# Kernel tuning notes

Measured on AMD Instinct MI355X. Metric: run time of the kernel, lower is better.

## Reference

```python
import jax, jax.numpy as jnp
import numpy as np

N_NODES = 50000
N_EDGES = 800000
D_IN = 128
D_H = 128


def setup_inputs() -> dict:
    key = jax.random.key(0)
    ks = jax.random.split(key, 16)
    s = 0.05
    return {
        "x": jax.random.normal(ks[0], (N_NODES, D_IN), dtype=jnp.float32),
        "edge_index": jax.random.randint(ks[1], (2, N_EDGES), 0, N_NODES, dtype=jnp.int64),
        # GraphConv 1: out = aggr(x_j) @ W_rel + b + x @ W_root (lin_root has no bias in PyG)
        "W1_rel": jax.random.normal(ks[2], (D_IN, D_H), dtype=jnp.float32) * s,
        "b1": jnp.zeros((D_H,), dtype=jnp.float32),
        "W1_root": jax.random.normal(ks[3], (D_IN, D_H), dtype=jnp.float32) * s,
        # GraphConv 2
        "W2_rel": jax.random.normal(ks[4], (D_H, D_H), dtype=jnp.float32) * s,
        "b2": jnp.zeros((D_H,), dtype=jnp.float32),
        "W2_root": jax.random.normal(ks[5], (D_H, D_H), dtype=jnp.float32) * s,
        # mean head MLP: Linear(2H->H), ReLU, Linear(H->1)
        "Wm1": jax.random.normal(ks[6], (2 * D_H, D_H), dtype=jnp.float32) * s,
        "bm1": jnp.zeros((D_H,), dtype=jnp.float32),
        "Wm2": jax.random.normal(ks[7], (D_H, 1), dtype=jnp.float32) * s,
        "bm2": jnp.zeros((1,), dtype=jnp.float32),
        # logvar head MLP
        "Wv1": jax.random.normal(ks[8], (2 * D_H, D_H), dtype=jnp.float32) * s,
        "bv1": jnp.zeros((D_H,), dtype=jnp.float32),
        "Wv2": jax.random.normal(ks[9], (D_H, 1), dtype=jnp.float32) * s,
        "bv2": jnp.zeros((1,), dtype=jnp.float32),
    }


def _graph_conv(h, src, dst, n, W_rel, b, W_root):
    # PyG GraphConv (aggr='add'): out_i = (sum_{j->i} h_j) @ W_rel + b + h_i @ W_root
    agg = jax.ops.segment_sum(h[src], dst, num_segments=n)
    return agg @ W_rel + b + h @ W_root


def reference(x, edge_index, W1_rel, b1, W1_root, W2_rel, b2, W2_root,
              Wm1, bm1, Wm2, bm2, Wv1, bv1, Wv2, bv2):
    n = x.shape[0]
    src, dst = edge_index[0], edge_index[1]
    h = jax.nn.relu(_graph_conv(x, src, dst, n, W1_rel, b1, W1_root))
    h = jax.nn.relu(_graph_conv(h, src, dst, n, W2_rel, b2, W2_root))
    combined = jnp.concatenate([h[src], h[dst]], axis=1)  # [E, 2H]
    mean = jax.nn.relu(combined @ Wm1 + bm1) @ Wm2 + bm2  # [E, 1]
    logvar = jax.nn.relu(combined @ Wv1 + bv1) @ Wv2 + bv2
    var = jnp.exp(0.5 * logvar)
    return (mean, var)
```

## Files before the change

### kernel.cpp

```cpp
#include <hip/hip_runtime.h>
#include <cstdint>

#define NF 128

typedef unsigned int uint;
typedef short bf16x8 __attribute__((ext_vector_type(8)));
typedef float f32x4  __attribute__((ext_vector_type(4)));

__device__ __forceinline__ float2 ld2(const float* p) {
    return *reinterpret_cast<const float2*>(p);
}
__device__ __forceinline__ float bflo(uint u) { return __uint_as_float(u << 16); }
__device__ __forceinline__ float bfhi(uint u) { return __uint_as_float(u & 0xffff0000u); }
__device__ __forceinline__ uint f2bf_rne(float f) {
    uint u = __float_as_uint(f);
    return (u + 0x7fffu + ((u >> 16) & 1u)) >> 16;
}
__device__ __forceinline__ uint pack2bf(float a, float b) {
    return f2bf_rne(a) | (f2bf_rne(b) << 16);
}

__device__ __forceinline__ bf16x8 ldfrag(const uint* __restrict__ tab, int idx, int kb, int g) {
    const uint4 u = *reinterpret_cast<const uint4*>(&tab[(size_t)idx * 64 + kb * 16 + g * 4]);
    union { uint4 u4; bf16x8 b; } c; c.u4 = u; return c.b;
}

__global__ __launch_bounds__(256) void cast_bf16_k(const float* __restrict__ in,
                                                   uint* __restrict__ out, int npairs)
{
    int i = blockIdx.x * 256 + threadIdx.x;
    if (i >= npairs) return;
    float2 v = ld2(&in[(size_t)i * 2]);
    out[i] = pack2bf(v.x, v.y);
}

struct W8 {
    const float* src[8];
    uint*        dst[8];
};
__global__ __launch_bounds__(256) void wtpack_k(W8 p)
{
    int m = blockIdx.y;
    const float* s = p.src[m];
    uint* d = p.dst[m];
    int idx = blockIdx.x * 256 + threadIdx.x;
    int c   = idx >> 6;
    int kdw = idx & 63;
    float a = s[(size_t)(2 * kdw)     * NF + c];
    float b = s[(size_t)(2 * kdw + 1) * NF + c];
    d[(size_t)c * 64 + kdw] = pack2bf(a, b);
}

__global__ __launch_bounds__(256) void count_k(const int* __restrict__ ei,
                                               int* __restrict__ deg, int E)
{
    int e = blockIdx.x * 256 + threadIdx.x;
    if (e >= E) return;
    atomicAdd(&deg[ei[E + e]], 1);
}

__global__ __launch_bounds__(256) void scan1_k(const int* __restrict__ deg,
                                               int* __restrict__ rowptr,
                                               int* __restrict__ bsum, int N)
{
    int i = blockIdx.x * 256 + threadIdx.x;
    int v = (i < N) ? deg[i] : 0;
    int lane = threadIdx.x & 63;
    int wid  = threadIdx.x >> 6;
    int x = v;
#pragma unroll
    for (int off = 1; off < 64; off <<= 1) {
        int y = __shfl_up(x, off);
        if (lane >= off) x += y;
    }
    __shared__ int wsum[4];
    if (lane == 63) wsum[wid] = x;
    __syncthreads();
    int wadd = 0;
#pragma unroll
    for (int w = 0; w < 4; ++w) wadd += (w < wid) ? wsum[w] : 0;
    int incl = x + wadd;
    if (i < N) rowptr[i] = incl - v;
    if (threadIdx.x == 255) bsum[blockIdx.x] = incl;
}

__global__ __launch_bounds__(256) void scan2_k(int* __restrict__ bsum, int NB)
{
    int i = threadIdx.x;
    int v = (i < NB) ? bsum[i] : 0;
    int lane = threadIdx.x & 63;
    int wid  = threadIdx.x >> 6;
    int x = v;
#pragma unroll
    for (int off = 1; off < 64; off <<= 1) {
        int y = __shfl_up(x, off);
        if (lane >= off) x += y;
    }
    __shared__ int wsum[4];
    if (lane == 63) wsum[wid] = x;
    __syncthreads();
    int wadd = 0;
#pragma unroll
    for (int w = 0; w < 4; ++w) wadd += (w < wid) ? wsum[w] : 0;
    int incl = x + wadd;
    __syncthreads();
    if (i < NB) bsum[i] = incl - v;
}

__global__ __launch_bounds__(256) void scan3_k(const int* __restrict__ bsum,
                                               int* __restrict__ rowptr,
                                               int* __restrict__ cursor, int N, int E)
{
    int i = blockIdx.x * 256 + threadIdx.x;
    if (i == 0) rowptr[N] = E;
    if (i >= N) return;
    int r = rowptr[i] + bsum[blockIdx.x];
    rowptr[i] = r;
    cursor[i] = r;
}

__global__ __launch_bounds__(256) void fill_k(const int* __restrict__ ei,
                                              int* __restrict__ cursor,
                                              int* __restrict__ srclist,
                                              int* __restrict__ invpos, int E)
{
    int e = blockIdx.x * 256 + threadIdx.x;
    if (e >= E) return;
    int s = ei[e];
    int d = ei[E + e];
    int pos = atomicAdd(&cursor[d], 1);
    srclist[pos] = s;
    invpos[e] = pos;
}

__global__ __launch_bounds__(256) void agg2_k(const uint* __restrict__ Xb,
                                              const int* __restrict__ rowptr,
                                              const int* __restrict__ srclist,
                                              uint* __restrict__ AGGb, int N)
{
    int gid   = blockIdx.x * 256 + threadIdx.x;
    int wave  = gid >> 6;
    int lane  = gid & 63;
    int half  = lane >> 5;
    int hlane = lane & 31;
    int node  = wave * 2 + half;
    int nc    = min(node, N - 1);
    int beg = rowptr[nc];
    int end = rowptr[nc + 1];
    if (node >= N) { beg = 0; end = 0; }

    float ax = 0.f, ay = 0.f, az = 0.f, aw = 0.f;
    float bx = 0.f, by = 0.f, bz = 0.f, bw = 0.f;

    uint2 w0 = make_uint2(0, 0), w1 = make_uint2(0, 0);
    int ok1 = 0;
    if (beg < end) {
        int s0 = srclist[beg];
        ok1 = (beg + 1 < end);
        int s1 = ok1 ? srclist[beg + 1] : s0;
        w0 = *reinterpret_cast<const uint2*>(&Xb[(size_t)s0 * 64 + hlane * 2]);
        w1 = *reinterpret_cast<const uint2*>(&Xb[(size_t)s1 * 64 + hlane * 2]);
    }
    for (int j = beg; j < end; j += 2) {
        int jn = j + 2;
        uint2 nw0 = w0, nw1 = w1;
        int nok1 = 0;
        if (jn < end) {
            int s0 = srclist[jn];
            nok1 = (jn + 1 < end);
            int s1 = nok1 ? srclist[jn + 1] : s0;
            nw0 = *reinterpret_cast<const uint2*>(&Xb[(size_t)s0 * 64 + hlane * 2]);
            nw1 = *reinterpret_cast<const uint2*>(&Xb[(size_t)s1 * 64 + hlane * 2]);
        }
        ax += bflo(w0.x); ay += bfhi(w0.x); az += bflo(w0.y); aw += bfhi(w0.y);
        if (ok1) { bx += bflo(w1.x); by += bfhi(w1.x); bz += bflo(w1.y); bw += bfhi(w1.y); }
        w0 = nw0; w1 = nw1; ok1 = nok1;
    }
    if (node < N) {
        uint2 o;
        o.x = pack2bf(ax + bx, ay + by);
        o.y = pack2bf(az + bz, aw + bw);
        *reinterpret_cast<uint2*>(&AGGb[(size_t)node * 64 + hlane * 2]) = o;
    }
}

__global__ __launch_bounds__(256) void dualgemm_mfma_k(
    const uint* __restrict__ Aa, const uint* __restrict__ WaT,
    const uint* __restrict__ Ab, const uint* __restrict__ WbT,
    const float* __restrict__ bias, uint* __restrict__ C, int Nrows)
{
    const int lane = threadIdx.x & 63;
    const int wid  = threadIdx.x >> 6;
    const int g    = lane >> 4;
    const int r15  = lane & 15;
    const int rowBase = blockIdx.x * 128 + wid * 32;
    if (rowBase >= Nrows) return;
    const int arow0 = rowBase + r15;
    const int t1ok  = (rowBase + 16) < Nrows;
    const int arow1 = t1ok ? (rowBase + 16 + r15) : arow0;

    bf16x8 ba0[4], bb0[4], ba1[4], bb1[4];
#pragma unroll
    for (int kb = 0; kb < 4; ++kb) {
        ba0[kb] = ldfrag(Aa, arow0, kb, g);
        bb0[kb] = ldfrag(Ab, arow0, kb, g);
        ba1[kb] = ldfrag(Aa, arow1, kb, g);
        bb1[kb] = ldfrag(Ab, arow1, kb, g);
    }

#pragma unroll
    for (int ct = 0; ct < 8; ++ct) {
        const int wcol = ct * 16 + r15;
        f32x4 a0 = {0.f, 0.f, 0.f, 0.f};
        f32x4 a1 = {0.f, 0.f, 0.f, 0.f};
#pragma unroll
        for (int kb = 0; kb < 4; ++kb) {
            bf16x8 wf = ldfrag(WaT, wcol, kb, g);
            a0 = __builtin_amdgcn_mfma_f32_16x16x32_bf16(wf, ba0[kb], a0, 0, 0, 0);
            a1 = __builtin_amdgcn_mfma_f32_16x16x32_bf16(wf, ba1[kb], a1, 0, 0, 0);
        }
#pragma unroll
        for (int kb = 0; kb < 4; ++kb) {
            bf16x8 wf = ldfrag(WbT, wcol, kb, g);
            a0 = __builtin_amdgcn_mfma_f32_16x16x32_bf16(wf, bb0[kb], a0, 0, 0, 0);
            a1 = __builtin_amdgcn_mfma_f32_16x16x32_bf16(wf, bb1[kb], a1, 0, 0, 0);
        }

        const int colBase = ct * 16 + g * 4;
        float4 bs = *reinterpret_cast<const float4*>(&bias[colBase]);
        uint2 pk0, pk1;
        pk0.x = pack2bf(fmaxf(a0[0] + bs.x, 0.f), fmaxf(a0[1] + bs.y, 0.f));
        pk0.y = pack2bf(fmaxf(a0[2] + bs.z, 0.f), fmaxf(a0[3] + bs.w, 0.f));
        pk1.x = pack2bf(fmaxf(a1[0] + bs.x, 0.f), fmaxf(a1[1] + bs.y, 0.f));
        pk1.y = pack2bf(fmaxf(a1[2] + bs.z, 0.f), fmaxf(a1[3] + bs.w, 0.f));
        *reinterpret_cast<uint2*>(&C[(size_t)arow0 * 64 + ct * 8 + g * 2]) = pk0;
        if (t1ok)
            *reinterpret_cast<uint2*>(&C[(size_t)arow1 * 64 + ct * 8 + g * 2]) = pk1;
    }
}

__global__ __launch_bounds__(256) void headgemm_mfma_k(
    const uint* __restrict__ Hb,
    const uint* __restrict__ WPt, const uint* __restrict__ WQt,
    const uint* __restrict__ WRt, const uint* __restrict__ WSt,
    const float* __restrict__ bm1, const float* __restrict__ bv1,
    uint* __restrict__ PRb, uint* __restrict__ QSb, int Nrows)
{
    const int lane = threadIdx.x & 63;
    const int wid  = threadIdx.x >> 6;
    const int g    = lane >> 4;
    const int r15  = lane & 15;
    const int rowBase = blockIdx.x * 128 + wid * 32;
    if (rowBase >= Nrows) return;
    const int arow0 = rowBase + r15;
    const int t1ok  = (rowBase + 16) < Nrows;
    const int arow1 = t1ok ? (rowBase + 16 + r15) : arow0;

    bf16x8 hb0[4], hb1[4];
#pragma unroll
    for (int kb = 0; kb < 4; ++kb) {
        hb0[kb] = ldfrag(Hb, arow0, kb, g);
        hb1[kb] = ldfrag(Hb, arow1, kb, g);
    }

#pragma unroll
    for (int ct = 0; ct < 8; ++ct) {
        const int wcol = ct * 16 + r15;
        f32x4 aP0 = {0.f,0.f,0.f,0.f}, aQ0 = {0.f,0.f,0.f,0.f};
        f32x4 aR0 = {0.f,0.f,0.f,0.f}, aS0 = {0.f,0.f,0.f,0.f};
        f32x4 aP1 = {0.f,0.f,0.f,0.f}, aQ1 = {0.f,0.f,0.f,0.f};
        f32x4 aR1 = {0.f,0.f,0.f,0.f}, aS1 = {0.f,0.f,0.f,0.f};
#pragma unroll
        for (int kb = 0; kb < 4; ++kb) {
            bf16x8 wP = ldfrag(WPt, wcol, kb, g);
            bf16x8 wQ = ldfrag(WQt, wcol, kb, g);
            bf16x8 wR = ldfrag(WRt, wcol, kb, g);
            bf16x8 wS = ldfrag(WSt, wcol, kb, g);
            aP0 = __builtin_amdgcn_mfma_f32_16x16x32_bf16(wP, hb0[kb], aP0, 0, 0, 0);
            aP1 = __builtin_amdgcn_mfma_f32_16x16x32_bf16(wP, hb1[kb], aP1, 0, 0, 0);
            aQ0 = __builtin_amdgcn_mfma_f32_16x16x32_bf16(wQ, hb0[kb], aQ0, 0, 0, 0);
            aQ1 = __builtin_amdgcn_mfma_f32_16x16x32_bf16(wQ, hb1[kb], aQ1, 0, 0, 0);
            aR0 = __builtin_amdgcn_mfma_f32_16x16x32_bf16(wR, hb0[kb], aR0, 0, 0, 0);
            aR1 = __builtin_amdgcn_mfma_f32_16x16x32_bf16(wR, hb1[kb], aR1, 0, 0, 0);
            aS0 = __builtin_amdgcn_mfma_f32_16x16x32_bf16(wS, hb0[kb], aS0, 0, 0, 0);
            aS1 = __builtin_amdgcn_mfma_f32_16x16x32_bf16(wS, hb1[kb], aS1, 0, 0, 0);
        }
        const int colBase = ct * 16 + g * 4;
        float4 bmv = *reinterpret_cast<const float4*>(&bm1[colBase]);
        float4 bvv = *reinterpret_cast<const float4*>(&bv1[colBase]);
        uint4 pr0, qs0, pr1, qs1;
        pr0.x = pack2bf(aP0[0] + bmv.x, aP0[1] + bmv.y);
        pr0.y = pack2bf(aR0[0] + bvv.x, aR0[1] + bvv.y);
        pr0.z = pack2bf(aP0[2] + bmv.z, aP0[3] + bmv.w);
        pr0.w = pack2bf(aR0[2] + bvv.z, aR0[3] + bvv.w);
        qs0.x = pack2bf(aQ0[0], aQ0[1]); qs0.y = pack2bf(aS0[0], aS0[1]);
        qs0.z = pack2bf(aQ0[2], aQ0[3]); qs0.w = pack2bf(aS0[2], aS0[3]);
        pr1.x = pack2bf(aP1[0] + bmv.x, aP1[1] + bmv.y);
        pr1.y = pack2bf(aR1[0] + bvv.x, aR1[1] + bvv.y);
        pr1.z = pack2bf(aP1[2] + bmv.z, aP1[3] + bmv.w);
        pr1.w = pack2bf(aR1[2] + bvv.z, aR1[3] + bvv.w);
        qs1.x = pack2bf(aQ1[0], aQ1[1]); qs1.y = pack2bf(aS1[0], aS1[1]);
        qs1.z = pack2bf(aQ1[2], aQ1[3]); qs1.w = pack2bf(aS1[2], aS1[3]);
        *reinterpret_cast<uint4*>(&PRb[(size_t)arow0 * 128 + ct * 16 + g * 4]) = pr0;
        *reinterpret_cast<uint4*>(&QSb[(size_t)arow0 * 128 + ct * 16 + g * 4]) = qs0;
        if (t1ok) {
            *reinterpret_cast<uint4*>(&PRb[(size_t)arow1 * 128 + ct * 16 + g * 4]) = pr1;
            *reinterpret_cast<uint4*>(&QSb[(size_t)arow1 * 128 + ct * 16 + g * 4]) = qs1;
        }
    }
}

__global__ __launch_bounds__(256) void edge_head3_k(
    const uint* __restrict__ PRb, const uint* __restrict__ QSb,
    const int* __restrict__ rowptr, const int* __restrict__ srclist,
    const float* __restrict__ Wm2, const float* __restrict__ Wv2,
    float2* __restrict__ tmp, int N)
{
    int gid   = blockIdx.x * 256 + threadIdx.x;
    int node  = gid >> 6;
    int lane  = gid & 63;
    int half  = lane >> 5;
    int hlane = lane & 31;
    if (node >= N) return;
    int beg = rowptr[node];
    int end = rowptr[node + 1];
    if (beg == end) return;

    uint4 qs4 = *reinterpret_cast<const uint4*>(&QSb[(size_t)node * 128 + hlane * 4]);
    float q0 = bflo(qs4.x), q1 = bfhi(qs4.x);
    float s0 = bflo(qs4.y), s1 = bfhi(qs4.y);
    float q2 = bflo(qs4.z), q3 = bfhi(qs4.z);
    float s2 = bflo(qs4.w), s3 = bfhi(qs4.w);

    float4 wm = *reinterpret_cast<const float4*>(&Wm2[hlane * 4]);
    float4 wv = *reinterpret_cast<const float4*>(&Wv2[hlane * 4]);

    int p0 = beg + half;
    int src0 = srclist[min(p0, end - 1)];
    uint4 pr_cur = *reinterpret_cast<const uint4*>(&PRb[(size_t)src0 * 128 + hlane * 4]);

    for (int base = beg; base < end; base += 2) {
        int p = base + half;
        uint4 pr_next = pr_cur;
        if (base + 2 < end) {
            int pn = base + 2 + half;
            int srcn = srclist[min(pn, end - 1)];
            pr_next = *reinterpret_cast<const uint4*>(&PRb[(size_t)srcn * 128 + hlane * 4]);
        }

        float P0 = bflo(pr_cur.x), P1 = bfhi(pr_cur.x);
        float R0 = bflo(pr_cur.y), R1 = bfhi(pr_cur.y);
        float P2 = bflo(pr_cur.z), P3 = bfhi(pr_cur.z);
        float R2 = bflo(pr_cur.w), R3 = bfhi(pr_cur.w);

        float pm = fmaf(fmaxf(P0 + q0, 0.f), wm.x,
                   fmaf(fmaxf(P1 + q1, 0.f), wm.y,
                   fmaf(fmaxf(P2 + q2, 0.f), wm.z,
                        fmaxf(P3 + q3, 0.f) * wm.w)));
        float pv = fmaf(fmaxf(R0 + s0, 0.f), wv.x,
                   fmaf(fmaxf(R1 + s1, 0.f), wv.y,
                   fmaf(fmaxf(R2 + s2, 0.f), wv.z,
                        fmaxf(R3 + s3, 0.f) * wv.w)));

        pm += __shfl_xor(pm, 16);
        pv += __shfl_xor(pv, 16);
        float c = (hlane & 16) ? pv : pm;
        c += __shfl_xor(c, 8);
        c += __shfl_xor(c, 4);
        c += __shfl_xor(c, 2);
        c += __shfl_xor(c, 1);
        float other = __shfl(c, (lane & 32) + 16);
        if (hlane == 0 && p < end) tmp[p] = make_float2(c, other);

        pr_cur = pr_next;
    }
}

__global__ __launch_bounds__(256) void permute_k(
    const float2* __restrict__ tmp, const int* __restrict__ invpos,
    const float* __restrict__ bm2, const float* __restrict__ bv2,
    float* __restrict__ mean_out, float* __restrict__ var_out, int E)
{
    int e = blockIdx.x * 256 + threadIdx.x;
    if (e >= E) return;
    float2 t = tmp[invpos[e]];
    mean_out[e] = t.x + bm2[0];
    var_out[e]  = expf(0.5f * (t.y + bv2[0]));
}

extern "C" void kernel_launch(void* const* d_in, const int* in_sizes, int n_in,
                              void* d_out, int out_size, void* d_ws, size_t ws_size,
                              hipStream_t stream)
{
    const float* x       = (const float*)d_in[0];
    const int*   ei      = (const int*)d_in[1];
    const float* W1_rel  = (const float*)d_in[2];
    const float* b1      = (const float*)d_in[3];
    const float* W1_root = (const float*)d_in[4];
    const float* W2_rel  = (const float*)d_in[5];
    const float* b2      = (const float*)d_in[6];
    const float* W2_root = (const float*)d_in[7];
    const float* Wm1     = (const float*)d_in[8];
    const float* bm1     = (const float*)d_in[9];
    const float* Wm2     = (const float*)d_in[10];
    const float* bm2     = (const float*)d_in[11];
    const float* Wv1     = (const float*)d_in[12];
    const float* bv1     = (const float*)d_in[13];
    const float* Wv2     = (const float*)d_in[14];
    const float* bv2     = (const float*)d_in[15];

    const int N = in_sizes[0] / NF;
    const int E = in_sizes[1] / 2;

    const size_t SZ16 = (size_t)N * NF * 2;

    char* base = (char*)d_ws;
    uint* x_b  = (uint*)(base);
    uint* h2b  = (uint*)(base);
    uint* h1b  = (uint*)(base + SZ16);
    uint* AGGb = (uint*)(base + 2 * SZ16);
    uint* PRb  = (uint*)(base + SZ16);
    uint* QSb  = (uint*)(base + 3 * SZ16);

    char* wts = base + 5 * SZ16;
    uint* wt[8];
    for (int i = 0; i < 8; ++i) wt[i] = (uint*)(wts + (size_t)i * 32768);

    char* csr = wts + 8 * 32768;
    int* deg     = (int*)(csr);
    int* rowptr  = (int*)(csr + (size_t)(N + 64) * 4);
    int* cursor  = (int*)(csr + (size_t)(N + 64) * 8);
    int* srclist = (int*)(csr + (size_t)(N + 64) * 12);
    int* invpos  = srclist + E;
    float2* tmp  = (float2*)(invpos + E);
    int* bsum    = (int*)(tmp + E);

    float* out_mean = (float*)d_out;
    float* out_var  = out_mean + E;

    dim3 blk(256);
    dim3 eGrid((E + 255) / 256);
    dim3 mfmaGrid((N + 127) / 128);
    dim3 nodeGrid((unsigned)(((size_t)N * 64 + 255) / 256));
    dim3 node2Grid((unsigned)((((size_t)(N + 1) / 2) * 64 + 255) / 256));
    const int NB = (N + 255) / 256;
    dim3 scanGrid(NB);

    hipLaunchKernelGGL(cast_bf16_k, nodeGrid, blk, 0, stream, x, x_b, N * 64);

    W8 wp;
    wp.src[0] = W1_rel;            wp.dst[0] = wt[0];
    wp.src[1] = W1_root;           wp.dst[1] = wt[1];
    wp.src[2] = W2_rel;            wp.dst[2] = wt[2];
    wp.src[3] = W2_root;           wp.dst[3] = wt[3];
    wp.src[4] = Wm1;               wp.dst[4] = wt[4];
    wp.src[5] = Wm1 + NF * NF;     wp.dst[5] = wt[5];
    wp.src[6] = Wv1;               wp.dst[6] = wt[6];
    wp.src[7] = Wv1 + NF * NF;     wp.dst[7] = wt[7];
    hipLaunchKernelGGL(wtpack_k, dim3(32, 8), blk, 0, stream, wp);

    hipMemsetAsync(deg, 0, (size_t)N * 4, stream);
    hipLaunchKernelGGL(count_k, eGrid, blk, 0, stream, ei, deg, E);
    hipLaunchKernelGGL(scan1_k, scanGrid, blk, 0, stream, deg, rowptr, bsum, N);
    hipLaunchKernelGGL(scan2_k, dim3(1), blk, 0, stream, bsum, NB);
    hipLaunchKernelGGL(scan3_k, scanGrid, blk, 0, stream, bsum, rowptr, cursor, N, E);
    hipLaunchKernelGGL(fill_k, eGrid, blk, 0, stream, ei, cursor, srclist, invpos, E);

    hipLaunchKernelGGL(agg2_k, node2Grid, blk, 0, stream, x_b, rowptr, srclist, AGGb, N);
    hipLaunchKernelGGL(dualgemm_mfma_k, mfmaGrid, blk, 0, stream,
                       AGGb, wt[0], x_b, wt[1], b1, h1b, N);

    hipLaunchKernelGGL(agg2_k, node2Grid, blk, 0, stream, h1b, rowptr, srclist, AGGb, N);
    hipLaunchKernelGGL(dualgemm_mfma_k, mfmaGrid, blk, 0, stream,
                       AGGb, wt[2], h1b, wt[3], b2, h2b, N);

    hipLaunchKernelGGL(headgemm_mfma_k, mfmaGrid, blk, 0, stream,
                       h2b, wt[4], wt[5], wt[6], wt[7], bm1, bv1, PRb, QSb, N);

    hipLaunchKernelGGL(edge_head3_k, nodeGrid, blk, 0, stream,
                       PRb, QSb, rowptr, srclist, Wm2, Wv2, tmp, N);

    hipLaunchKernelGGL(permute_k, eGrid, blk, 0, stream,
                       tmp, invpos, bm2, bv2, out_mean, out_var, E);
}
```

Measured before the change: 450.4 us.

## Fuse prologue kernels, merge scan passes, and fuse conv2 GEMM into head GEMM

Merges the x cast, weight packing and degree counting into one prologue launch. The scan's second and third passes become one kernel in which each block recomputes its prefix from the block sums. The second GraphConv GEMM now keeps its bf16 output tile in LDS and feeds it straight into the head GEMM, so h2 is never written to or read back from global memory. This removes several launches and a full node-feature round trip, at the cost of more LDS per block and somewhat redundant per-block prefix sums.

```diff
diff --git a/kernel.cpp b/kernel.cpp
--- a/kernel.cpp
+++ b/kernel.cpp
@@ -25,38 +25,38 @@
     union { uint4 u4; bf16x8 b; } c; c.u4 = u; return c.b;
 }
 
-__global__ __launch_bounds__(256) void cast_bf16_k(const float* __restrict__ in,
-                                                   uint* __restrict__ out, int npairs)
-{
-    int i = blockIdx.x * 256 + threadIdx.x;
-    if (i >= npairs) return;
-    float2 v = ld2(&in[(size_t)i * 2]);
-    out[i] = pack2bf(v.x, v.y);
-}
-
 struct W8 {
     const float* src[8];
     uint*        dst[8];
 };
-__global__ __launch_bounds__(256) void wtpack_k(W8 p)
-{
-    int m = blockIdx.y;
-    const float* s = p.src[m];
-    uint* d = p.dst[m];
-    int idx = blockIdx.x * 256 + threadIdx.x;
-    int c   = idx >> 6;
-    int kdw = idx & 63;
-    float a = s[(size_t)(2 * kdw)     * NF + c];
-    float b = s[(size_t)(2 * kdw + 1) * NF + c];
-    d[(size_t)c * 64 + kdw] = pack2bf(a, b);
-}
-
-__global__ __launch_bounds__(256) void count_k(const int* __restrict__ ei,
-                                               int* __restrict__ deg, int E)
-{
-    int e = blockIdx.x * 256 + threadIdx.x;
-    if (e >= E) return;
-    atomicAdd(&deg[ei[E + e]], 1);
+__global__ __launch_bounds__(256) void prologue_k(
+    const float* __restrict__ x, uint* __restrict__ x_b, int npairs, int castBlocks,
+    W8 wp,
+    const int* __restrict__ ei, int* __restrict__ deg, int E, int countBlocks)
+{
+    int b = blockIdx.x;
+    if (b < castBlocks) {
+        int i = b * 256 + threadIdx.x;
+        if (i >= npairs) return;
+        float2 v = ld2(&x[(size_t)i * 2]);
+        x_b[i] = pack2bf(v.x, v.y);
+    } else if (b < castBlocks + 256) {
+        int wb = b - castBlocks;
+        int m  = wb >> 5;
+        int bx = wb & 31;
+        const float* s = wp.src[m];
+        uint* d = wp.dst[m];
+        int idx = bx * 256 + threadIdx.x;
+        int c   = idx >> 6;
+        int kdw = idx & 63;
+        float a  = s[(size_t)(2 * kdw)     * NF + c];
+        float b2 = s[(size_t)(2 * kdw + 1) * NF + c];
+        d[(size_t)c * 64 + kdw] = pack2bf(a, b2);
+    } else {
+        int e = (b - castBlocks - 256) * 256 + threadIdx.x;
+        if (e >= E) return;
+        atomicAdd(&deg[ei[E + e]], 1);
+    }
 }
 
 __global__ __launch_bounds__(256) void scan1_k(const int* __restrict__ deg,
@@ -84,37 +84,25 @@
     if (threadIdx.x == 255) bsum[blockIdx.x] = incl;
 }
 
-__global__ __launch_bounds__(256) void scan2_k(int* __restrict__ bsum, int NB)
-{
-    int i = threadIdx.x;
-    int v = (i < NB) ? bsum[i] : 0;
-    int lane = threadIdx.x & 63;
-    int wid  = threadIdx.x >> 6;
-    int x = v;
-#pragma unroll
-    for (int off = 1; off < 64; off <<= 1) {
-        int y = __shfl_up(x, off);
-        if (lane >= off) x += y;
-    }
-    __shared__ int wsum[4];
-    if (lane == 63) wsum[wid] = x;
+__global__ __launch_bounds__(256) void scan23_k(const int* __restrict__ bsum,
+                                                int* __restrict__ rowptr,
+                                                int* __restrict__ cursor, int N, int E)
+{
+    int tid = threadIdx.x;
+    int v = (tid < blockIdx.x) ? bsum[tid] : 0;
+    int lane = tid & 63;
+    int wid  = tid >> 6;
+#pragma unroll
+    for (int off = 32; off > 0; off >>= 1) v += __shfl_xor(v, off);
+    __shared__ int ws[4];
+    if (lane == 0) ws[wid] = v;
     __syncthreads();
-    int wadd = 0;
-#pragma unroll
-    for (int w = 0; w < 4; ++w) wadd += (w < wid) ? wsum[w] : 0;
-    int incl = x + wadd;
-    __syncthreads();
-    if (i < NB) bsum[i] = incl - v;
-}
-
-__global__ __launch_bounds__(256) void scan3_k(const int* __restrict__ bsum,
-                                               int* __restrict__ rowptr,
-                                               int* __restrict__ cursor, int N, int E)
-{
-    int i = blockIdx.x * 256 + threadIdx.x;
-    if (i == 0) rowptr[N] = E;
+    int prefix = ws[0] + ws[1] + ws[2] + ws[3];
+
+    if (blockIdx.x == 0 && tid == 0) rowptr[N] = E;
+    int i = blockIdx.x * 256 + tid;
     if (i >= N) return;
-    int r = rowptr[i] + bsum[blockIdx.x];
+    int r = rowptr[i] + prefix;
     rowptr[i] = r;
     cursor[i] = r;
 }
@@ -239,28 +227,78 @@
     }
 }
 
-__global__ __launch_bounds__(256) void headgemm_mfma_k(
-    const uint* __restrict__ Hb,
+#define LROW 72
+__global__ __launch_bounds__(256) void conv2head_k(
+    const uint* __restrict__ Aa, const uint* __restrict__ WaT,
+    const uint* __restrict__ Ab, const uint* __restrict__ WbT,
+    const float* __restrict__ bias,
     const uint* __restrict__ WPt, const uint* __restrict__ WQt,
     const uint* __restrict__ WRt, const uint* __restrict__ WSt,
     const float* __restrict__ bm1, const float* __restrict__ bv1,
     uint* __restrict__ PRb, uint* __restrict__ QSb, int Nrows)
 {
+    __shared__ uint h2s[128 * LROW];
+
     const int lane = threadIdx.x & 63;
     const int wid  = threadIdx.x >> 6;
     const int g    = lane >> 4;
     const int r15  = lane & 15;
     const int rowBase = blockIdx.x * 128 + wid * 32;
-    if (rowBase >= Nrows) return;
+    const int active = rowBase < Nrows;
     const int arow0 = rowBase + r15;
-    const int t1ok  = (rowBase + 16) < Nrows;
-    const int arow1 = t1ok ? (rowBase + 16 + r15) : arow0;
-
+    const int t1ok  = active && ((rowBase + 16) < Nrows);
+    const int arow1 = t1ok ? (rowBase + 16 + r15) : (active ? arow0 : 0);
+    const int lrow0 = wid * 32 + r15;
+    const int lrow1 = wid * 32 + 16 + r15;
+
+    if (active) {
+        bf16x8 ba0[4], bb0[4], ba1[4], bb1[4];
+#pragma unroll
+        for (int kb = 0; kb < 4; ++kb) {
+            ba0[kb] = ldfrag(Aa, arow0, kb, g);
+            bb0[kb] = ldfrag(Ab, arow0, kb, g);
+            ba1[kb] = ldfrag(Aa, arow1, kb, g);
+            bb1[kb] = ldfrag(Ab, arow1, kb, g);
+        }
+#pragma unroll
+        for (int ct = 0; ct < 8; ++ct) {
+            const int wcol = ct * 16 + r15;
+            f32x4 a0 = {0.f, 0.f, 0.f, 0.f};
+            f32x4 a1 = {0.f, 0.f, 0.f, 0.f};
+#pragma unroll
+            for (int kb = 0; kb < 4; ++kb) {
+                bf16x8 wf = ldfrag(WaT, wcol, kb, g);
+                a0 = __builtin_amdgcn_mfma_f32_16x16x32_bf16(wf, ba0[kb], a0, 0, 0, 0);
+                a1 = __builtin_amdgcn_mfma_f32_16x16x32_bf16(wf, ba1[kb], a1, 0, 0, 0);
+            }
+#pragma unroll
+            for (int kb = 0; kb < 4; ++kb) {
+                bf16x8 wf = ldfrag(WbT, wcol, kb, g);
+                a0 = __builtin_amdgcn_mfma_f32_16x16x32_bf16(wf, bb0[kb], a0, 0, 0, 0);
+                a1 = __builtin_amdgcn_mfma_f32_16x16x32_bf16(wf, bb1[kb], a1, 0, 0, 0);
+            }
+            const int colBase = ct * 16 + g * 4;
+            float4 bs = *reinterpret_cast<const float4*>(&bias[colBase]);
+            uint2 pk0, pk1;
+            pk0.x = pack2bf(fmaxf(a0[0] + bs.x, 0.f), fmaxf(a0[1] + bs.y, 0.f));
+            pk0.y = pack2bf(fmaxf(a0[2] + bs.z, 0.f), fmaxf(a0[3] + bs.w, 0.f));
+            pk1.x = pack2bf(fmaxf(a1[0] + bs.x, 0.f), fmaxf(a1[1] + bs.y, 0.f));
+            pk1.y = pack2bf(fmaxf(a1[2] + bs.z, 0.f), fmaxf(a1[3] + bs.w, 0.f));
+            *reinterpret_cast<uint2*>(&h2s[lrow0 * LROW + ct * 8 + g * 2]) = pk0;
+            *reinterpret_cast<uint2*>(&h2s[lrow1 * LROW + ct * 8 + g * 2]) = pk1;
+        }
+    }
+    __syncthreads();
+
+    if (!active) return;
     bf16x8 hb0[4], hb1[4];
 #pragma unroll
     for (int kb = 0; kb < 4; ++kb) {
-        hb0[kb] = ldfrag(Hb, arow0, kb, g);
-        hb1[kb] = ldfrag(Hb, arow1, kb, g);
+        union { uint4 u4; bf16x8 b; } c0, c1;
+        c0.u4 = *reinterpret_cast<const uint4*>(&h2s[lrow0 * LROW + kb * 16 + g * 4]);
+        c1.u4 = *reinterpret_cast<const uint4*>(&h2s[lrow1 * LROW + kb * 16 + g * 4]);
+        hb0[kb] = c0.b;
+        hb1[kb] = c1.b;
     }
 
 #pragma unroll
@@ -416,7 +454,6 @@
 
     char* base = (char*)d_ws;
     uint* x_b  = (uint*)(base);
-    uint* h2b  = (uint*)(base);
     uint* h1b  = (uint*)(base + SZ16);
     uint* AGGb = (uint*)(base + 2 * SZ16);
     uint* PRb  = (uint*)(base + SZ16);
@@ -439,14 +476,15 @@
     float* out_var  = out_mean + E;
 
     dim3 blk(256);
-    dim3 eGrid((E + 255) / 256);
+    const int castBlocks  = (N * 64 + 255) / 256;
+    const int countBlocks = (E + 255) / 256;
+    dim3 proGrid(castBlocks + 256 + countBlocks);
+    dim3 eGrid(countBlocks);
     dim3 mfmaGrid((N + 127) / 128);
     dim3 nodeGrid((unsigned)(((size_t)N * 64 + 255) / 256));
     dim3 node2Grid((unsigned)((((size_t)(N + 1) / 2) * 64 + 255) / 256));
     const int NB = (N + 255) / 256;
     dim3 scanGrid(NB);
-
-    hipLaunchKernelGGL(cast_bf16_k, nodeGrid, blk, 0, stream, x, x_b, N * 64);
 
     W8 wp;
     wp.src[0] = W1_rel;            wp.dst[0] = wt[0];
@@ -457,13 +495,13 @@
     wp.src[5] = Wm1 + NF * NF;     wp.dst[5] = wt[5];
     wp.src[6] = Wv1;               wp.dst[6] = wt[6];
     wp.src[7] = Wv1 + NF * NF;     wp.dst[7] = wt[7];
-    hipLaunchKernelGGL(wtpack_k, dim3(32, 8), blk, 0, stream, wp);
 
     hipMemsetAsync(deg, 0, (size_t)N * 4, stream);
-    hipLaunchKernelGGL(count_k, eGrid, blk, 0, stream, ei, deg, E);
+    hipLaunchKernelGGL(prologue_k, proGrid, blk, 0, stream,
+                       x, x_b, N * 64, castBlocks, wp, ei, deg, E, countBlocks);
+
     hipLaunchKernelGGL(scan1_k, scanGrid, blk, 0, stream, deg, rowptr, bsum, N);
-    hipLaunchKernelGGL(scan2_k, dim3(1), blk, 0, stream, bsum, NB);
-    hipLaunchKernelGGL(scan3_k, scanGrid, blk, 0, stream, bsum, rowptr, cursor, N, E);
+    hipLaunchKernelGGL(scan23_k, scanGrid, blk, 0, stream, bsum, rowptr, cursor, N, E);
     hipLaunchKernelGGL(fill_k, eGrid, blk, 0, stream, ei, cursor, srclist, invpos, E);
 
     hipLaunchKernelGGL(agg2_k, node2Grid, blk, 0, stream, x_b, rowptr, srclist, AGGb, N);
@@ -471,11 +509,9 @@
                        AGGb, wt[0], x_b, wt[1], b1, h1b, N);
 
     hipLaunchKernelGGL(agg2_k, node2Grid, blk, 0, stream, h1b, rowptr, srclist, AGGb, N);
-    hipLaunchKernelGGL(dualgemm_mfma_k, mfmaGrid, blk, 0, stream,
-                       AGGb, wt[2], h1b, wt[3], b2, h2b, N);
-
-    hipLaunchKernelGGL(headgemm_mfma_k, mfmaGrid, blk, 0, stream,
-                       h2b, wt[4], wt[5], wt[6], wt[7], bm1, bv1, PRb, QSb, N);
+    hipLaunchKernelGGL(conv2head_k, mfmaGrid, blk, 0, stream,
+                       AGGb, wt[2], h1b, wt[3], b2,
+                       wt[4], wt[5], wt[6], wt[7], bm1, bv1, PRb, QSb, N);
 
     hipLaunchKernelGGL(edge_head3_k, nodeGrid, blk, 0, stream,
                        PRb, QSb, rowptr, srclist, Wm2, Wv2, tmp, N);
```

After: 440.0 us. 1.02x faster.
